# Kernel optimization log

Measured on AMD Instinct MI355X. Metric: run time of the kernel, lower is better.

The kernel has to match this reference:

```python
import jax, jax.numpy as jnp
from jax import lax
import numpy as np

WIN = 11
SIGMA = 1.5
VAL_RANGE = 10.0
C1 = (0.01 * VAL_RANGE) ** 2
C2 = (0.03 * VAL_RANGE) ** 2


def _gauss_window():
    # matches pytorch-ssim create_window: normalized 1D gaussian, outer product
    g = np.exp(-((np.arange(WIN) - WIN // 2) ** 2) / (2.0 * SIGMA ** 2))
    g = g / g.sum()
    return jnp.asarray(np.outer(g, g), jnp.float32)


def _blur(x, win):
    # depthwise 11x11 gaussian conv, padding=0 (VALID), per pytorch-ssim with padd=0
    k = x.shape[1]
    kern = jnp.broadcast_to(win[None, None], (k, 1, WIN, WIN)).astype(x.dtype)
    return lax.conv_general_dilated(x, kern, (1, 1), 'VALID', feature_group_count=k)


def setup_inputs() -> dict:
    key = jax.random.key(0)
    ks = jax.random.split(key, 7)
    B, C, H, W = 8, 64, 256, 256
    x = jax.random.normal(ks[0], (B, C, H, W), jnp.float32)
    mask = jax.random.randint(ks[1], (B, H, W), 0, 2, jnp.int32)
    conv_w = jax.random.normal(ks[2], (1, 3, 3, 1), jnp.float32) * 0.3
    w1 = jax.random.normal(ks[3], (C, C), jnp.float32) * (1.0 / np.sqrt(C))
    b1 = jax.random.normal(ks[4], (C,), jnp.float32) * 0.01
    w2 = jax.random.normal(ks[5], (C, C), jnp.float32) * (1.0 / np.sqrt(C))
    b2 = jax.random.normal(ks[6], (C,), jnp.float32) * 0.01
    return {'x': x, 'mask': mask, 'conv_w': conv_w, 'w1': w1, 'b1': b1, 'w2': w2, 'b2': b2}


def reference(x, mask, conv_w, w1, b1, w2, b2):
    B, C, H, W = x.shape
    m = mask.astype(x.dtype)[:, None]  # [B,1,H,W]

    # ChannelPool: max/mean/min over channel dim -> [B,3,H,W]
    xc = jnp.stack([x.max(axis=1), x.mean(axis=1), x.min(axis=1)], axis=1)

    # ChannelNorm: masked per-sample, per-channel mean / unbiased std; zero outside mask
    n = m.sum(axis=(2, 3), keepdims=True)                       # [B,1,1,1]
    mean = (xc * m).sum(axis=(2, 3), keepdims=True) / n
    var = (((xc - mean) ** 2) * m).sum(axis=(2, 3), keepdims=True) / (n - 1.0)
    xf = (xc - mean) / jnp.sqrt(var) * m                        # [B,3,H,W]

    # Pairwise SSIM between xf channels (3) and x channels (C), vectorized
    win = _gauss_window()
    mu_f = _blur(xf, win)                                       # [B,3,H',W']
    mu_x = _blur(x, win)                                        # [B,C,H',W']
    ef2 = _blur(xf * xf, win)
    ex2 = _blur(x * x, win)
    prod = (xf[:, :, None] * x[:, None]).reshape(B, 3 * C, H, W)
    Hp, Wp = H - WIN + 1, W - WIN + 1
    exf = _blur(prod, win).reshape(B, 3, C, Hp, Wp)

    mu1 = mu_f[:, :, None]                                      # [B,3,1,H',W']
    mu2 = mu_x[:, None]                                         # [B,1,C,H',W']
    s1 = ef2[:, :, None] - mu1 ** 2
    s2 = ex2[:, None] - mu2 ** 2
    s12 = exf - mu1 * mu2
    ssim_map = ((2 * mu1 * mu2 + C1) * (2 * s12 + C2)) / ((mu1 ** 2 + mu2 ** 2 + C1) * (s1 + s2 + C2))
    ssim_info = ssim_map.mean(axis=(3, 4))                      # [B,3,C]

    # spatial Conv2d(3,1,(3,1),pad=(1,0)) on [B,3,C,1], then ReLU, MLP, Sigmoid
    h = lax.conv_general_dilated(ssim_info[..., None], conv_w, (1, 1), ((1, 1), (0, 0)))
    h = jax.nn.relu(h).reshape(B, C)
    h = jax.nn.relu(h @ w1.T + b1)
    h = jax.nn.sigmoid(h @ w2.T + b2)
    return h, ssim_info
```

## Files before the change

kernel.cpp:

```cpp
#include <hip/hip_runtime.h>
#include <cmath>

#define Bn   8
#define Cn   64
#define HWc  65536
#define HPc  246
#define HPWPc 60516
#define C1v  0.01f
#define C2v  0.09f
#define VPITCH 224

static __device__ __forceinline__ void gauss11(float* gw) {
    double gg[11]; double s = 0.0;
#pragma unroll
    for (int j = 0; j < 11; ++j) { double d = (double)(j - 5); gg[j] = exp(-(d * d) / 4.5); s += gg[j]; }
#pragma unroll
    for (int j = 0; j < 11; ++j) gw[j] = (float)(gg[j] / s);
}

static __device__ __forceinline__ float4 f4z() { return make_float4(0.f, 0.f, 0.f, 0.f); }
static __device__ __forceinline__ float4 f4scale(float g, const float4 v) {
    return make_float4(g * v.x, g * v.y, g * v.z, g * v.w);
}
static __device__ __forceinline__ void f4add(float4& a, const float4 v) {
    a.x += v.x; a.y += v.y; a.z += v.z; a.w += v.w;
}
static __device__ __forceinline__ void f4fma(float4& a, const float4 u, const float4 v) {
    a.x = fmaf(u.x, v.x, a.x); a.y = fmaf(u.y, v.y, a.y);
    a.z = fmaf(u.z, v.z, a.z); a.w = fmaf(u.w, v.w, a.w);
}

static __device__ __forceinline__ float wave_sum64(float v) {
    v += __int_as_float(__builtin_amdgcn_update_dpp(0, __float_as_int(v), 0x111, 0xf, 0xf, true));
    v += __int_as_float(__builtin_amdgcn_update_dpp(0, __float_as_int(v), 0x112, 0xf, 0xf, true));
    v += __int_as_float(__builtin_amdgcn_update_dpp(0, __float_as_int(v), 0x114, 0xf, 0xf, true));
    v += __int_as_float(__builtin_amdgcn_update_dpp(0, __float_as_int(v), 0x118, 0xf, 0xf, true));
    v += __int_as_float(__builtin_amdgcn_update_dpp(0, __float_as_int(v), 0x142, 0xf, 0xf, true));
    v += __int_as_float(__builtin_amdgcn_update_dpp(0, __float_as_int(v), 0x143, 0xf, 0xf, true));
    return v;
}

__global__ __launch_bounds__(256) void k1_stats(const float* __restrict__ x, const int* __restrict__ mask,
                                                float* __restrict__ xcf, float* __restrict__ stats) {
    const int b = blockIdx.y;
    const int p0 = blockIdx.x * 1024 + threadIdx.x * 4;
    const float4* xp = (const float4*)(x + (size_t)b * Cn * HWc) + (p0 >> 2);
    float4 v = xp[0];
    float4 vmax = v, vmin = v, vsum = v;
#pragma unroll 4
    for (int c = 1; c < Cn; ++c) {
        float4 u = xp[(size_t)c * (HWc / 4)];
        vmax.x = fmaxf(vmax.x, u.x); vmax.y = fmaxf(vmax.y, u.y);
        vmax.z = fmaxf(vmax.z, u.z); vmax.w = fmaxf(vmax.w, u.w);
        vmin.x = fminf(vmin.x, u.x); vmin.y = fminf(vmin.y, u.y);
        vmin.z = fminf(vmin.z, u.z); vmin.w = fminf(vmin.w, u.w);
        vsum.x += u.x; vsum.y += u.y; vsum.z += u.z; vsum.w += u.w;
    }
    float4 vmean = make_float4(vsum.x * (1.f / 64.f), vsum.y * (1.f / 64.f),
                               vsum.z * (1.f / 64.f), vsum.w * (1.f / 64.f));
    *(float4*)(xcf + (size_t)(b * 3 + 0) * HWc + p0) = vmax;
    *(float4*)(xcf + (size_t)(b * 3 + 1) * HWc + p0) = vmean;
    *(float4*)(xcf + (size_t)(b * 3 + 2) * HWc + p0) = vmin;
    int4 mv = *(const int4*)(mask + (size_t)b * HWc + p0);
    float m0 = (float)mv.x, m1 = (float)mv.y, m2 = (float)mv.z, m3 = (float)mv.w;
    float r[7];
    r[0] = m0 + m1 + m2 + m3;
    r[1] = vmax.x * m0 + vmax.y * m1 + vmax.z * m2 + vmax.w * m3;
    r[2] = vmean.x * m0 + vmean.y * m1 + vmean.z * m2 + vmean.w * m3;
    r[3] = vmin.x * m0 + vmin.y * m1 + vmin.z * m2 + vmin.w * m3;
    r[4] = vmax.x * vmax.x * m0 + vmax.y * vmax.y * m1 + vmax.z * vmax.z * m2 + vmax.w * vmax.w * m3;
    r[5] = vmean.x * vmean.x * m0 + vmean.y * vmean.y * m1 + vmean.z * vmean.z * m2 + vmean.w * vmean.w * m3;
    r[6] = vmin.x * vmin.x * m0 + vmin.y * vmin.y * m1 + vmin.z * vmin.z * m2 + vmin.w * vmin.w * m3;
#pragma unroll
    for (int k = 0; k < 7; ++k) {
        float vv = wave_sum64(r[k]);
        if ((threadIdx.x & 63) == 63) atomicAdd(&stats[b * 8 + k], vv);
    }
}

__global__ __launch_bounds__(256) void k4_blur3(const float* __restrict__ xc, const int* __restrict__ mask,
                                                const float* __restrict__ stats,
                                                float* __restrict__ muf, float* __restrict__ ef2g) {
    __shared__ __align__(16) float vb2[32 * 92];
    const int t = threadIdx.x;
    const int bi = blockIdx.z, b = bi / 3, i = bi % 3;
    const int y0 = blockIdx.y * 32, x0 = blockIdx.x * 32;
    float gw[11]; gauss11(gw);
    const float nst = stats[b * 8 + 0];
    const float s1 = stats[b * 8 + 1 + i], s2 = stats[b * 8 + 4 + i];
    const float mean = s1 / nst;
    const float rstd = rsqrtf((s2 - s1 * s1 / nst) / (nst - 1.0f));
    if (t < 176) {
        const int rg = t / 11, cg = t % 11, colo = cg * 4;
        const int gcb = min(x0 + colo, 252);
        const float* xp = xc + (size_t)bi * HWc;
        const int* mp = mask + (size_t)b * HWc;
        float4 av0 = f4z(), ab0 = f4z(), av1 = f4z(), ab1 = f4z();
#pragma unroll
        for (int k = 0; k < 12; ++k) {
            int gr = min(y0 + 2 * rg + k, 255);
            float4 v = *(const float4*)(xp + gr * 256 + gcb);
            int4 mv = *(const int4*)(mp + gr * 256 + gcb);
            float4 f;
            f.x = (v.x - mean) * rstd * (float)mv.x;
            f.y = (v.y - mean) * rstd * (float)mv.y;
            f.z = (v.z - mean) * rstd * (float)mv.z;
            f.w = (v.w - mean) * rstd * (float)mv.w;
            if (k <= 10) { float4 tv = f4scale(gw[k], f); f4add(av0, tv); f4fma(ab0, tv, f); }
            if (k >= 1)  { float4 tv = f4scale(gw[k - 1], f); f4add(av1, tv); f4fma(ab1, tv, f); }
        }
        {
            float* dst = &vb2[(2 * rg + 0) * 92 + colo * 2];
            *(float4*)&dst[0] = make_float4(av0.x, ab0.x, av0.y, ab0.y);
            *(float4*)&dst[4] = make_float4(av0.z, ab0.z, av0.w, ab0.w);
        }
        {
            float* dst = &vb2[(2 * rg + 1) * 92 + colo * 2];
            *(float4*)&dst[0] = make_float4(av1.x, ab1.x, av1.y, ab1.y);
            *(float4*)&dst[4] = make_float4(av1.z, ab1.z, av1.w, ab1.w);
        }
    }
    __syncthreads();
    {
        const int erow = t >> 3, ecg = t & 7;
        const int oy = y0 + erow;
        const float* src = &vb2[erow * 92 + ecg * 8];
        float a00 = 0.f, a01 = 0.f, a02 = 0.f, a03 = 0.f;
        float a10 = 0.f, a11 = 0.f, a12 = 0.f, a13 = 0.f;
#pragma unroll
        for (int m = 0; m < 14; ++m) {
            float v0 = src[m * 2 + 0];
            float v1 = src[m * 2 + 1];
#pragma unroll
            for (int j = 0; j < 4; ++j) {
                const int kk = m - j;
                if (kk >= 0 && kk <= 10) {
                    if (j == 0) { a00 = fmaf(gw[kk], v0, a00); a10 = fmaf(gw[kk], v1, a10); }
                    if (j == 1) { a01 = fmaf(gw[kk], v0, a01); a11 = fmaf(gw[kk], v1, a11); }
                    if (j == 2) { a02 = fmaf(gw[kk], v0, a02); a12 = fmaf(gw[kk], v1, a12); }
                    if (j == 3) { a03 = fmaf(gw[kk], v0, a03); a13 = fmaf(gw[kk], v1, a13); }
                }
            }
        }
        if (oy < HPc) {
            size_t ob = (size_t)bi * HPWPc + (size_t)oy * HPc;
            int oxb = x0 + ecg * 4;
            if (oxb + 0 < HPc) { muf[ob + oxb + 0] = a00; ef2g[ob + oxb + 0] = a10; }
            if (oxb + 1 < HPc) { muf[ob + oxb + 1] = a01; ef2g[ob + oxb + 1] = a11; }
            if (oxb + 2 < HPc) { muf[ob + oxb + 2] = a02; ef2g[ob + oxb + 2] = a12; }
            if (oxb + 3 < HPc) { muf[ob + oxb + 3] = a03; ef2g[ob + oxb + 3] = a13; }
        }
    }
}

#define T(F,J,KK,V) h##F##_##J = fmaf(G##KK, (V), h##F##_##J);
#define TM0(F,V)  T(F,0,0,V)
#define TM1(F,V)  T(F,0,1,V) T(F,1,0,V)
#define TM2(F,V)  T(F,0,2,V) T(F,1,1,V) T(F,2,0,V)
#define TM3(F,V)  T(F,0,3,V) T(F,1,2,V) T(F,2,1,V) T(F,3,0,V)
#define TM4(F,V)  T(F,0,4,V) T(F,1,3,V) T(F,2,2,V) T(F,3,1,V)
#define TM5(F,V)  T(F,0,5,V) T(F,1,4,V) T(F,2,3,V) T(F,3,2,V)
#define TM6(F,V)  T(F,0,6,V) T(F,1,5,V) T(F,2,4,V) T(F,3,3,V)
#define TM7(F,V)  T(F,0,7,V) T(F,1,6,V) T(F,2,5,V) T(F,3,4,V)
#define TM8(F,V)  T(F,0,8,V) T(F,1,7,V) T(F,2,6,V) T(F,3,5,V)
#define TM9(F,V)  T(F,0,9,V) T(F,1,8,V) T(F,2,7,V) T(F,3,6,V)
#define TM10(F,V) T(F,0,10,V) T(F,1,9,V) T(F,2,8,V) T(F,3,7,V)
#define TM11(F,V) T(F,1,10,V) T(F,2,9,V) T(F,3,8,V)
#define TM12(F,V) T(F,2,10,V) T(F,3,9,V)
#define TM13(F,V) T(F,3,10,V)

#define DECLH(J) float h0_##J = 0.f, h1_##J = 0.f, h2_##J = 0.f, h3_##J = 0.f, h4_##J = 0.f;
#define DECLJ(J) float M0_##J, M1_##J, M2_##J, S0_##J, S1_##J, S2_##J;
#define SETI(I,J) { float mu1 = 0.f, e2 = 0.f; \
    if (vld) { size_t o = (size_t)(b * 3 + I) * HPWPc + (size_t)oy * HPc + ox; mu1 = muf[o]; e2 = ef2g[o]; } \
    M##I##_##J = mu1; S##I##_##J = vld ? ((e2 - mu1 * mu1) + C2v) : __builtin_inff(); }
#define SETJ(J) { int ox = ox0 + J; bool vld = (oy < HPc) && (ox < HPc); \
    SETI(0,J) SETI(1,J) SETI(2,J) }

#define SSIMI(I,J,HV) { float am = M##I##_##J * m2; \
    float num = fmaf(2.f, am, C1v) * fmaf(2.f, (HV) - am, C2v); \
    float den = fmaf(M##I##_##J, M##I##_##J, c1m2) * (S##I##_##J + s2); \
    sa##I += num * __builtin_amdgcn_rcpf(den); }
#define SSIMJ(J) { float m2 = h0_##J; float m2sq = m2 * m2; \
    float c1m2 = C1v + m2sq; float s2 = h1_##J - m2sq; \
    SSIMI(0,J,h2_##J) SSIMI(1,J,h3_##J) SSIMI(2,J,h4_##J) }

#define XROW(K) { int gr = y0 + 2 * vrg + (K); gr = (gr > 255) ? 255 : gr; \
    xv##K = *(const float4*)(xp + gr * 256 + gcb); }
#define XLOAD(CC) do { if (vact) { \
    int cc = (CC); if (cc > Cn - 1) cc = Cn - 1; \
    const float* xp = xb + (size_t)cc * HWc; \
    XROW(0) XROW(1) XROW(2) XROW(3) XROW(4) XROW(5) \
    XROW(6) XROW(7) XROW(8) XROW(9) XROW(10) XROW(11) \
} } while (0)

#define VSTEP(K, DOA, DOB, GA, GB) { \
    float4 xv = xv##K; \
    const int ro = (2 * vrg + (K)) * 44 + vcolo; \
    float4 f0 = *(const float4*)&f0in[ro]; \
    float4 f1v = *(const float4*)&f1in[ro]; \
    float4 f2v = *(const float4*)&f2in[ro]; \
    if (DOA) { float4 tv = f4scale((GA), xv); f4add(xA0, tv); f4fma(xQ0, tv, xv); \
               f4fma(p00, tv, f0); f4fma(p10, tv, f1v); f4fma(p20, tv, f2v); } \
    if (DOB) { float4 tv = f4scale((GB), xv); f4add(xA1, tv); f4fma(xQ1, tv, xv); \
               f4fma(p01, tv, f0); f4fma(p11, tv, f1v); f4fma(p21, tv, f2v); } }

#define VCOMP(BUF) do { if (vact) { \
    float4 xA0 = f4z(), xQ0 = f4z(), p00 = f4z(), p10 = f4z(), p20 = f4z(); \
    float4 xA1 = f4z(), xQ1 = f4z(), p01 = f4z(), p11 = f4z(), p21 = f4z(); \
    VSTEP(0, 1, 0, G0, G0)  VSTEP(1, 1, 1, G1, G0)  VSTEP(2, 1, 1, G2, G1) \
    VSTEP(3, 1, 1, G3, G2)  VSTEP(4, 1, 1, G4, G3)  VSTEP(5, 1, 1, G5, G4) \
    VSTEP(6, 1, 1, G6, G5)  VSTEP(7, 1, 1, G7, G6)  VSTEP(8, 1, 1, G8, G7) \
    VSTEP(9, 1, 1, G9, G8)  VSTEP(10, 1, 1, G10, G9) VSTEP(11, 0, 1, G0, G10) \
    { float* dst = &BUF[(2 * vrg + 0) * VPITCH + vcolo * 5]; \
      *(float4*)&dst[0]  = make_float4(xA0.x, xQ0.x, p00.x, p10.x); \
      *(float4*)&dst[4]  = make_float4(p20.x, xA0.y, xQ0.y, p00.y); \
      *(float4*)&dst[8]  = make_float4(p10.y, p20.y, xA0.z, xQ0.z); \
      *(float4*)&dst[12] = make_float4(p00.z, p10.z, p20.z, xA0.w); \
      *(float4*)&dst[16] = make_float4(xQ0.w, p00.w, p10.w, p20.w); } \
    { float* dst = &BUF[(2 * vrg + 1) * VPITCH + vcolo * 5]; \
      *(float4*)&dst[0]  = make_float4(xA1.x, xQ1.x, p01.x, p11.x); \
      *(float4*)&dst[4]  = make_float4(p21.x, xA1.y, xQ1.y, p01.y); \
      *(float4*)&dst[8]  = make_float4(p11.y, p21.y, xA1.z, xQ1.z); \
      *(float4*)&dst[12] = make_float4(p01.z, p11.z, p21.z, xA1.w); \
      *(float4*)&dst[16] = make_float4(xQ1.w, p01.w, p11.w, p21.w); } \
} } while (0)

#define HORIZ(CC, BUF) do { \
    const float* src = &BUF[erow * VPITCH + ecg * 20]; \
    DECLH(0) DECLH(1) DECLH(2) DECLH(3) \
    float4 L0 = *(const float4*)(src + 0); \
    TM0(0, L0.x) TM0(1, L0.y) TM0(2, L0.z) TM0(3, L0.w) \
    float4 L1 = *(const float4*)(src + 4); \
    TM0(4, L1.x) TM1(0, L1.y) TM1(1, L1.z) TM1(2, L1.w) \
    float4 L2 = *(const float4*)(src + 8); \
    TM1(3, L2.x) TM1(4, L2.y) TM2(0, L2.z) TM2(1, L2.w) \
    float4 L3 = *(const float4*)(src + 12); \
    TM2(2, L3.x) TM2(3, L3.y) TM2(4, L3.z) TM3(0, L3.w) \
    float4 L4 = *(const float4*)(src + 16); \
    TM3(1, L4.x) TM3(2, L4.y) TM3(3, L4.z) TM3(4, L4.w) \
    float4 L5 = *(const float4*)(src + 20); \
    TM4(0, L5.x) TM4(1, L5.y) TM4(2, L5.z) TM4(3, L5.w) \
    float4 L6 = *(const float4*)(src + 24); \
    TM4(4, L6.x) TM5(0, L6.y) TM5(1, L6.z) TM5(2, L6.w) \
    float4 L7 = *(const float4*)(src + 28); \
    TM5(3, L7.x) TM5(4, L7.y) TM6(0, L7.z) TM6(1, L7.w) \
    float4 L8 = *(const float4*)(src + 32); \
    TM6(2, L8.x) TM6(3, L8.y) TM6(4, L8.z) TM7(0, L8.w) \
    float4 L9 = *(const float4*)(src + 36); \
    TM7(1, L9.x) TM7(2, L9.y) TM7(3, L9.z) TM7(4, L9.w) \
    float4 L10 = *(const float4*)(src + 40); \
    TM8(0, L10.x) TM8(1, L10.y) TM8(2, L10.z) TM8(3, L10.w) \
    float4 L11 = *(const float4*)(src + 44); \
    TM8(4, L11.x) TM9(0, L11.y) TM9(1, L11.z) TM9(2, L11.w) \
    float4 L12 = *(const float4*)(src + 48); \
    TM9(3, L12.x) TM9(4, L12.y) TM10(0, L12.z) TM10(1, L12.w) \
    float4 L13 = *(const float4*)(src + 52); \
    TM10(2, L13.x) TM10(3, L13.y) TM10(4, L13.z) TM11(0, L13.w) \
    float4 L14 = *(const float4*)(src + 56); \
    TM11(1, L14.x) TM11(2, L14.y) TM11(3, L14.z) TM11(4, L14.w) \
    float4 L15 = *(const float4*)(src + 60); \
    TM12(0, L15.x) TM12(1, L15.y) TM12(2, L15.z) TM12(3, L15.w) \
    float4 L16 = *(const float4*)(src + 64); \
    TM12(4, L16.x) TM13(0, L16.y) TM13(1, L16.z) TM13(2, L16.w) \
    float4 L17 = *(const float4*)(src + 68); \
    TM13(3, L17.x) TM13(4, L17.y) \
    float sa0 = 0.f, sa1 = 0.f, sa2 = 0.f; \
    SSIMJ(0) SSIMJ(1) SSIMJ(2) SSIMJ(3) \
    sa0 = wave_sum64(sa0); \
    sa1 = wave_sum64(sa1); \
    sa2 = wave_sum64(sa2); \
    if ((t & 63) == 63) { \
        atomicAdd(&ssum[(b * 3 + 0) * 64 + (CC)], sa0); \
        atomicAdd(&ssum[(b * 3 + 1) * 64 + (CC)], sa1); \
        atomicAdd(&ssum[(b * 3 + 2) * 64 + (CC)], sa2); \
    } \
} while (0)

__global__ __launch_bounds__(256, 2) void k5_main(const float* __restrict__ x, const float* __restrict__ xc,
                                                  const int* __restrict__ mask, const float* __restrict__ stats,
                                                  const float* __restrict__ muf, const float* __restrict__ ef2g,
                                                  float* __restrict__ ssum) {
    __shared__ __align__(16) float f0in[42 * 44];
    __shared__ __align__(16) float f1in[42 * 44];
    __shared__ __align__(16) float f2in[42 * 44];
    __shared__ __align__(16) float vb5[32 * VPITCH];
    const int t = threadIdx.x;
    const int b = blockIdx.z;
    const int y0 = blockIdx.y * 32, x0 = blockIdx.x * 32;
    const double e0 = exp(-25.0 / 4.5), e1 = exp(-16.0 / 4.5), e2d = exp(-9.0 / 4.5),
                 e3 = exp(-4.0 / 4.5), e4 = exp(-1.0 / 4.5);
    const double sg = 1.0 + 2.0 * (e0 + e1 + e2d + e3 + e4);
    const float G0 = (float)(e0 / sg), G1 = (float)(e1 / sg), G2 = (float)(e2d / sg),
                G3 = (float)(e3 / sg), G4 = (float)(e4 / sg), G5 = (float)(1.0 / sg);
    const float G6 = G4, G7 = G3, G8 = G2, G9 = G1, G10 = G0;
    const float nst = stats[b * 8 + 0];
    const float s1a = stats[b * 8 + 1], s2a = stats[b * 8 + 4];
    const float s1b = stats[b * 8 + 2], s2b = stats[b * 8 + 5];
    const float s1c = stats[b * 8 + 3], s2c = stats[b * 8 + 6];
    const float mean0 = s1a / nst, rstd0 = rsqrtf((s2a - s1a * s1a / nst) / (nst - 1.0f));
    const float mean1 = s1b / nst, rstd1 = rsqrtf((s2b - s1b * s1b / nst) / (nst - 1.0f));
    const float mean2 = s1c / nst, rstd2 = rsqrtf((s2c - s1c * s1c / nst) / (nst - 1.0f));
    for (int q = t; q < 42 * 11; q += 256) {
        int row = q / 11, cg = q % 11;
        int gr = min(y0 + row, 255), gc = min(x0 + cg * 4, 252);
        int go = gr * 256 + gc;
        int lo = row * 44 + cg * 4;
        int4 mv = *(const int4*)(mask + (size_t)b * HWc + go);
        float m0 = (float)mv.x, m1 = (float)mv.y, m2 = (float)mv.z, m3 = (float)mv.w;
        float4 v0 = *(const float4*)(xc + (size_t)(b * 3 + 0) * HWc + go);
        v0.x = (v0.x - mean0) * rstd0 * m0; v0.y = (v0.y - mean0) * rstd0 * m1;
        v0.z = (v0.z - mean0) * rstd0 * m2; v0.w = (v0.w - mean0) * rstd0 * m3;
        *(float4*)&f0in[lo] = v0;
        float4 v1 = *(const float4*)(xc + (size_t)(b * 3 + 1) * HWc + go);
        v1.x = (v1.x - mean1) * rstd1 * m0; v1.y = (v1.y - mean1) * rstd1 * m1;
        v1.z = (v1.z - mean1) * rstd1 * m2; v1.w = (v1.w - mean1) * rstd1 * m3;
        *(float4*)&f1in[lo] = v1;
        float4 v2 = *(const float4*)(xc + (size_t)(b * 3 + 2) * HWc + go);
        v2.x = (v2.x - mean2) * rstd2 * m0; v2.y = (v2.y - mean2) * rstd2 * m1;
        v2.z = (v2.z - mean2) * rstd2 * m2; v2.w = (v2.w - mean2) * rstd2 * m3;
        *(float4*)&f2in[lo] = v2;
    }
    const int erow = t >> 3, ecg = t & 7;
    const int oy = y0 + erow;
    const int ox0 = x0 + ecg * 4;
    DECLJ(0) DECLJ(1) DECLJ(2) DECLJ(3)
    SETJ(0) SETJ(1) SETJ(2) SETJ(3)
    const float* xb = x + (size_t)b * Cn * HWc;
    const int vrg = t / 11, vcg = t % 11, vcolo = vcg * 4;
    const int gcb = min(x0 + vcolo, 252);
    const bool vact = (t < 176);
    float4 xv0, xv1, xv2, xv3, xv4, xv5, xv6, xv7, xv8, xv9, xv10, xv11;

    XLOAD(0);
    __syncthreads();
#pragma unroll 1
    for (int c = 0; c < Cn; ++c) {
        VCOMP(vb5);
        XLOAD(c + 1);
        __syncthreads();
        HORIZ(c, vb5);
        __syncthreads();
    }
}

__global__ __launch_bounds__(512) void k6_head(const float* __restrict__ ssum, const float* __restrict__ cw,
                                               const float* __restrict__ w1, const float* __restrict__ b1,
                                               const float* __restrict__ w2, const float* __restrict__ b2,
                                               float* __restrict__ out) {
    __shared__ float si[1536];
    __shared__ float h0[512];
    __shared__ float h1[512];
    const int t = threadIdx.x;
    const float inv = 1.0f / (float)HPWPc;
    for (int idx = t; idx < 1536; idx += 512) {
        float v = ssum[idx] * inv;
        si[idx] = v;
        out[512 + idx] = v;
    }
    __syncthreads();
    const int b = t >> 6, y = t & 63;
    float acc = 0.f;
#pragma unroll
    for (int i = 0; i < 3; ++i) {
#pragma unroll
        for (int kh = 0; kh < 3; ++kh) {
            int yy = y + kh - 1;
            if (yy >= 0 && yy < 64) acc = fmaf(si[(b * 3 + i) * 64 + yy], cw[i * 3 + kh], acc);
        }
    }
    h0[t] = fmaxf(acc, 0.f);
    __syncthreads();
    float a1 = b1[y];
    for (int c = 0; c < 64; ++c) a1 = fmaf(h0[(b << 6) + c], w1[(y << 6) + c], a1);
    h1[t] = fmaxf(a1, 0.f);
    __syncthreads();
    float a2 = b2[y];
    for (int c = 0; c < 64; ++c) a2 = fmaf(h1[(b << 6) + c], w2[(y << 6) + c], a2);
    out[t] = 1.f / (1.f + expf(-a2));
}

extern "C" void kernel_launch(void* const* d_in, const int* in_sizes, int n_in,
                              void* d_out, int out_size, void* d_ws, size_t ws_size,
                              hipStream_t stream) {
    const float* x      = (const float*)d_in[0];
    const int*   mask   = (const int*)d_in[1];
    const float* conv_w = (const float*)d_in[2];
    const float* w1     = (const float*)d_in[3];
    const float* b1     = (const float*)d_in[4];
    const float* w2     = (const float*)d_in[5];
    const float* b2     = (const float*)d_in[6];
    float* out = (float*)d_out;

    float* wsf   = (float*)d_ws;
    float* stats = wsf;
    float* ssum  = wsf + 64;
    float* xcf   = wsf + 1600;
    float* muf   = xcf + (size_t)Bn * 3 * HWc;
    float* ef2   = muf + (size_t)Bn * 3 * HPWPc;

    hipMemsetAsync(d_ws, 0, 6400, stream);

    k1_stats<<<dim3(64, 8), 256, 0, stream>>>(x, mask, xcf, stats);
    k4_blur3<<<dim3(8, 8, 24), 256, 0, stream>>>(xcf, mask, stats, muf, ef2);
    k5_main<<<dim3(8, 8, 8), 256, 0, stream>>>(x, xcf, mask, stats, muf, ef2, ssum);
    k6_head<<<1, 512, 0, stream>>>(ssum, conv_w, w1, b1, w2, b2, out);
}
```

Before: 643.7 us.

## Fuse normalized-feature blur kernel into main SSIM kernel via shared memory

Removes the separate k4_blur3 launch that blurred the three normalized pooled channels and wrote mu_f and E[f^2] to global memory. k5_main now computes those blurs itself from the normalized tiles it already stages in shared memory, reusing its vertical/horizontal blur buffer before the channel loop. This drops a kernel launch and the global write and read of the intermediate maps. In exchange each block does extra blur work and barriers before its main loop, and the register load in k5_main rises.

```diff
diff --git a/kernel.cpp b/kernel.cpp
--- a/kernel.cpp
+++ b/kernel.cpp
@@ -9,14 +9,6 @@
 #define C1v  0.01f
 #define C2v  0.09f
 #define VPITCH 224
-
-static __device__ __forceinline__ void gauss11(float* gw) {
-    double gg[11]; double s = 0.0;
-#pragma unroll
-    for (int j = 0; j < 11; ++j) { double d = (double)(j - 5); gg[j] = exp(-(d * d) / 4.5); s += gg[j]; }
-#pragma unroll
-    for (int j = 0; j < 11; ++j) gw[j] = (float)(gg[j] / s);
-}
 
 static __device__ __forceinline__ float4 f4z() { return make_float4(0.f, 0.f, 0.f, 0.f); }
 static __device__ __forceinline__ float4 f4scale(float g, const float4 v) {
@@ -78,81 +70,6 @@
     }
 }
 
-__global__ __launch_bounds__(256) void k4_blur3(const float* __restrict__ xc, const int* __restrict__ mask,
-                                                const float* __restrict__ stats,
-                                                float* __restrict__ muf, float* __restrict__ ef2g) {
-    __shared__ __align__(16) float vb2[32 * 92];
-    const int t = threadIdx.x;
-    const int bi = blockIdx.z, b = bi / 3, i = bi % 3;
-    const int y0 = blockIdx.y * 32, x0 = blockIdx.x * 32;
-    float gw[11]; gauss11(gw);
-    const float nst = stats[b * 8 + 0];
-    const float s1 = stats[b * 8 + 1 + i], s2 = stats[b * 8 + 4 + i];
-    const float mean = s1 / nst;
-    const float rstd = rsqrtf((s2 - s1 * s1 / nst) / (nst - 1.0f));
-    if (t < 176) {
-        const int rg = t / 11, cg = t % 11, colo = cg * 4;
-        const int gcb = min(x0 + colo, 252);
-        const float* xp = xc + (size_t)bi * HWc;
-        const int* mp = mask + (size_t)b * HWc;
-        float4 av0 = f4z(), ab0 = f4z(), av1 = f4z(), ab1 = f4z();
-#pragma unroll
-        for (int k = 0; k < 12; ++k) {
-            int gr = min(y0 + 2 * rg + k, 255);
-            float4 v = *(const float4*)(xp + gr * 256 + gcb);
-            int4 mv = *(const int4*)(mp + gr * 256 + gcb);
-            float4 f;
-            f.x = (v.x - mean) * rstd * (float)mv.x;
-            f.y = (v.y - mean) * rstd * (float)mv.y;
-            f.z = (v.z - mean) * rstd * (float)mv.z;
-            f.w = (v.w - mean) * rstd * (float)mv.w;
-            if (k <= 10) { float4 tv = f4scale(gw[k], f); f4add(av0, tv); f4fma(ab0, tv, f); }
-            if (k >= 1)  { float4 tv = f4scale(gw[k - 1], f); f4add(av1, tv); f4fma(ab1, tv, f); }
-        }
-        {
-            float* dst = &vb2[(2 * rg + 0) * 92 + colo * 2];
-            *(float4*)&dst[0] = make_float4(av0.x, ab0.x, av0.y, ab0.y);
-            *(float4*)&dst[4] = make_float4(av0.z, ab0.z, av0.w, ab0.w);
-        }
-        {
-            float* dst = &vb2[(2 * rg + 1) * 92 + colo * 2];
-            *(float4*)&dst[0] = make_float4(av1.x, ab1.x, av1.y, ab1.y);
-            *(float4*)&dst[4] = make_float4(av1.z, ab1.z, av1.w, ab1.w);
-        }
-    }
-    __syncthreads();
-    {
-        const int erow = t >> 3, ecg = t & 7;
-        const int oy = y0 + erow;
-        const float* src = &vb2[erow * 92 + ecg * 8];
-        float a00 = 0.f, a01 = 0.f, a02 = 0.f, a03 = 0.f;
-        float a10 = 0.f, a11 = 0.f, a12 = 0.f, a13 = 0.f;
-#pragma unroll
-        for (int m = 0; m < 14; ++m) {
-            float v0 = src[m * 2 + 0];
-            float v1 = src[m * 2 + 1];
-#pragma unroll
-            for (int j = 0; j < 4; ++j) {
-                const int kk = m - j;
-                if (kk >= 0 && kk <= 10) {
-                    if (j == 0) { a00 = fmaf(gw[kk], v0, a00); a10 = fmaf(gw[kk], v1, a10); }
-                    if (j == 1) { a01 = fmaf(gw[kk], v0, a01); a11 = fmaf(gw[kk], v1, a11); }
-                    if (j == 2) { a02 = fmaf(gw[kk], v0, a02); a12 = fmaf(gw[kk], v1, a12); }
-                    if (j == 3) { a03 = fmaf(gw[kk], v0, a03); a13 = fmaf(gw[kk], v1, a13); }
-                }
-            }
-        }
-        if (oy < HPc) {
-            size_t ob = (size_t)bi * HPWPc + (size_t)oy * HPc;
-            int oxb = x0 + ecg * 4;
-            if (oxb + 0 < HPc) { muf[ob + oxb + 0] = a00; ef2g[ob + oxb + 0] = a10; }
-            if (oxb + 1 < HPc) { muf[ob + oxb + 1] = a01; ef2g[ob + oxb + 1] = a11; }
-            if (oxb + 2 < HPc) { muf[ob + oxb + 2] = a02; ef2g[ob + oxb + 2] = a12; }
-            if (oxb + 3 < HPc) { muf[ob + oxb + 3] = a03; ef2g[ob + oxb + 3] = a13; }
-        }
-    }
-}
-
 #define T(F,J,KK,V) h##F##_##J = fmaf(G##KK, (V), h##F##_##J);
 #define TM0(F,V)  T(F,0,0,V)
 #define TM1(F,V)  T(F,0,1,V) T(F,1,0,V)
@@ -171,11 +88,6 @@
 
 #define DECLH(J) float h0_##J = 0.f, h1_##J = 0.f, h2_##J = 0.f, h3_##J = 0.f, h4_##J = 0.f;
 #define DECLJ(J) float M0_##J, M1_##J, M2_##J, S0_##J, S1_##J, S2_##J;
-#define SETI(I,J) { float mu1 = 0.f, e2 = 0.f; \
-    if (vld) { size_t o = (size_t)(b * 3 + I) * HPWPc + (size_t)oy * HPc + ox; mu1 = muf[o]; e2 = ef2g[o]; } \
-    M##I##_##J = mu1; S##I##_##J = vld ? ((e2 - mu1 * mu1) + C2v) : __builtin_inff(); }
-#define SETJ(J) { int ox = ox0 + J; bool vld = (oy < HPc) && (ox < HPc); \
-    SETI(0,J) SETI(1,J) SETI(2,J) }
 
 #define SSIMI(I,J,HV) { float am = M##I##_##J * m2; \
     float num = fmaf(2.f, am, C1v) * fmaf(2.f, (HV) - am, C2v); \
@@ -277,9 +189,54 @@
     } \
 } while (0)
 
+#define FSTEP(SRC, K, DOA, DOB, GA, GB) { \
+    float4 ff = *(const float4*)&SRC[(2 * vrg + (K)) * 44 + vcolo]; \
+    if (DOA) { float4 tv = f4scale((GA), ff); f4add(av0, tv); f4fma(ab0, tv, ff); } \
+    if (DOB) { float4 tv = f4scale((GB), ff); f4add(av1, tv); f4fma(ab1, tv, ff); } }
+
+#define VERTF(SRC) do { if (vact) { \
+    float4 av0 = f4z(), ab0 = f4z(), av1 = f4z(), ab1 = f4z(); \
+    FSTEP(SRC, 0, 1, 0, G0, G0)  FSTEP(SRC, 1, 1, 1, G1, G0)  FSTEP(SRC, 2, 1, 1, G2, G1) \
+    FSTEP(SRC, 3, 1, 1, G3, G2)  FSTEP(SRC, 4, 1, 1, G4, G3)  FSTEP(SRC, 5, 1, 1, G5, G4) \
+    FSTEP(SRC, 6, 1, 1, G6, G5)  FSTEP(SRC, 7, 1, 1, G7, G6)  FSTEP(SRC, 8, 1, 1, G8, G7) \
+    FSTEP(SRC, 9, 1, 1, G9, G8)  FSTEP(SRC, 10, 1, 1, G10, G9) FSTEP(SRC, 11, 0, 1, G0, G10) \
+    { float* dst = &vb5[(2 * vrg + 0) * VPITCH + vcolo * 2]; \
+      *(float4*)&dst[0] = make_float4(av0.x, ab0.x, av0.y, ab0.y); \
+      *(float4*)&dst[4] = make_float4(av0.z, ab0.z, av0.w, ab0.w); } \
+    { float* dst = &vb5[(2 * vrg + 1) * VPITCH + vcolo * 2]; \
+      *(float4*)&dst[0] = make_float4(av1.x, ab1.x, av1.y, ab1.y); \
+      *(float4*)&dst[4] = make_float4(av1.z, ab1.z, av1.w, ab1.w); } \
+} } while (0)
+
+#define HSETJ(I, J, AM, AE) { bool vld = (oy < HPc) && (ox0 + (J) < HPc); \
+    M##I##_##J = vld ? (AM) : 0.f; \
+    S##I##_##J = vld ? (((AE) - (AM) * (AM)) + C2v) : __builtin_inff(); }
+
+#define HORIZF(I) do { \
+    const float* hsrc = &vb5[erow * VPITCH + ecg * 8]; \
+    float a00 = 0.f, a01 = 0.f, a02 = 0.f, a03 = 0.f; \
+    float a10 = 0.f, a11 = 0.f, a12 = 0.f, a13 = 0.f; \
+    _Pragma("unroll") \
+    for (int m = 0; m < 14; ++m) { \
+        float v0 = hsrc[m * 2 + 0]; \
+        float v1 = hsrc[m * 2 + 1]; \
+        _Pragma("unroll") \
+        for (int j = 0; j < 4; ++j) { \
+            const int kk = m - j; \
+            if (kk >= 0 && kk <= 10) { \
+                float g = gwA[kk]; \
+                if (j == 0) { a00 = fmaf(g, v0, a00); a10 = fmaf(g, v1, a10); } \
+                if (j == 1) { a01 = fmaf(g, v0, a01); a11 = fmaf(g, v1, a11); } \
+                if (j == 2) { a02 = fmaf(g, v0, a02); a12 = fmaf(g, v1, a12); } \
+                if (j == 3) { a03 = fmaf(g, v0, a03); a13 = fmaf(g, v1, a13); } \
+            } \
+        } \
+    } \
+    HSETJ(I, 0, a00, a10) HSETJ(I, 1, a01, a11) HSETJ(I, 2, a02, a12) HSETJ(I, 3, a03, a13) \
+} while (0)
+
 __global__ __launch_bounds__(256, 2) void k5_main(const float* __restrict__ x, const float* __restrict__ xc,
                                                   const int* __restrict__ mask, const float* __restrict__ stats,
-                                                  const float* __restrict__ muf, const float* __restrict__ ef2g,
                                                   float* __restrict__ ssum) {
     __shared__ __align__(16) float f0in[42 * 44];
     __shared__ __align__(16) float f1in[42 * 44];
@@ -294,6 +251,7 @@
     const float G0 = (float)(e0 / sg), G1 = (float)(e1 / sg), G2 = (float)(e2d / sg),
                 G3 = (float)(e3 / sg), G4 = (float)(e4 / sg), G5 = (float)(1.0 / sg);
     const float G6 = G4, G7 = G3, G8 = G2, G9 = G1, G10 = G0;
+    const float gwA[11] = { G0, G1, G2, G3, G4, G5, G6, G7, G8, G9, G10 };
     const float nst = stats[b * 8 + 0];
     const float s1a = stats[b * 8 + 1], s2a = stats[b * 8 + 4];
     const float s1b = stats[b * 8 + 2], s2b = stats[b * 8 + 5];
@@ -325,14 +283,25 @@
     const int oy = y0 + erow;
     const int ox0 = x0 + ecg * 4;
     DECLJ(0) DECLJ(1) DECLJ(2) DECLJ(3)
-    SETJ(0) SETJ(1) SETJ(2) SETJ(3)
     const float* xb = x + (size_t)b * Cn * HWc;
     const int vrg = t / 11, vcg = t % 11, vcolo = vcg * 4;
     const int gcb = min(x0 + vcolo, 252);
     const bool vact = (t < 176);
     float4 xv0, xv1, xv2, xv3, xv4, xv5, xv6, xv7, xv8, xv9, xv10, xv11;
 
+    __syncthreads();
+    VERTF(f0in);
+    __syncthreads();
+    HORIZF(0);
+    __syncthreads();
+    VERTF(f1in);
+    __syncthreads();
+    HORIZF(1);
+    __syncthreads();
+    VERTF(f2in);
+    __syncthreads();
     XLOAD(0);
+    HORIZF(2);
     __syncthreads();
 #pragma unroll 1
     for (int c = 0; c < Cn; ++c) {
@@ -396,13 +365,10 @@
     float* stats = wsf;
     float* ssum  = wsf + 64;
     float* xcf   = wsf + 1600;
-    float* muf   = xcf + (size_t)Bn * 3 * HWc;
-    float* ef2   = muf + (size_t)Bn * 3 * HPWPc;
 
     hipMemsetAsync(d_ws, 0, 6400, stream);
 
     k1_stats<<<dim3(64, 8), 256, 0, stream>>>(x, mask, xcf, stats);
-    k4_blur3<<<dim3(8, 8, 24), 256, 0, stream>>>(xcf, mask, stats, muf, ef2);
-    k5_main<<<dim3(8, 8, 8), 256, 0, stream>>>(x, xcf, mask, stats, muf, ef2, ssum);
+    k5_main<<<dim3(8, 8, 8), 256, 0, stream>>>(x, xcf, mask, stats, ssum);
     k6_head<<<1, 512, 0, stream>>>(ssum, conv_w, w1, b1, w2, b2, out);
 }
```

New measurement: 630.1 us. -2.1%, faster.
